# Kernel tuning notes

Hardware: AMD Instinct MI355X
Metric: run time of the kernel (lower is better)

The kernel has to match this reference:

```python
import jax, jax.numpy as jnp
import numpy as np

C = 128          # channels
L = 2            # num_layers
NA = 30000       # nodes of type 'a'
NB = 30000       # nodes of type 'b'
E = 150000       # edges per edge type
SEED_SIZE = 1024
EPS = 1e-5


def _ln(x, g, b):
    # LayerNorm over last dim (biased variance, eps=1e-5), matches nn.LayerNorm / PyG LayerNorm(mode='node')
    m = x.mean(-1, keepdims=True)
    v = ((x - m) ** 2).mean(-1, keepdims=True)
    return (x - m) * jax.lax.rsqrt(v + EPS) * g + b


def _seg_mean(msg, dst, n):
    # PyG aggr='mean': mean of incoming messages, 0 for isolated nodes
    s = jax.ops.segment_sum(msg, dst, num_segments=n)
    cnt = jax.ops.segment_sum(jnp.ones((dst.shape[0],), msg.dtype), dst, num_segments=n)
    return s / jnp.maximum(cnt, 1.0)[:, None]


def _prmp_conv(x_src, x_dst, edge, w1, b1, w2, b2, g, be, uw, ub):
    src, dst = edge[0], edge[1]
    xi = x_dst[dst]                                   # [E, C] dst feats per edge
    xj = x_src[src]                                   # [E, C] src feats per edge
    h = jax.nn.relu(jax.lax.stop_gradient(xi) @ w1 + b1)  # pred_mlp on detached x_i
    pred = h @ w2 + b2
    msg = _ln(xj - pred, g, be)                       # LayerNorm(residual) per edge
    agg = _seg_mean(msg, dst, x_dst.shape[0])         # mean aggregation to dst nodes
    return jax.nn.relu(jnp.concatenate([x_dst, agg], -1) @ uw + ub)  # update_mlp


def setup_inputs() -> dict:
    key = jax.random.key(0)
    ks = jax.random.split(key, 12)
    edge_ab = jnp.stack([jax.random.randint(ks[2], (E,), 0, NA, jnp.int32),
                         jax.random.randint(ks[3], (E,), 0, NB, jnp.int32)])
    edge_ba = jnp.stack([jax.random.randint(ks[4], (E,), 0, NB, jnp.int32),
                         jax.random.randint(ks[5], (E,), 0, NA, jnp.int32)])
    return {
        "x_a": jax.random.normal(ks[0], (NA, C), jnp.float32),
        "x_b": jax.random.normal(ks[1], (NB, C), jnp.float32),
        "edge_ab": edge_ab,
        "edge_ba": edge_ba,
        "pred_w1": jax.random.normal(ks[6], (L, 2, C, C), jnp.float32) * 0.05,
        "pred_b1": jnp.zeros((L, 2, C), jnp.float32),
        "pred_w2": jax.random.normal(ks[7], (L, 2, C, C), jnp.float32) * 0.05,
        "pred_b2": jnp.zeros((L, 2, C), jnp.float32),
        "msg_gamma": jnp.ones((L, 2, C), jnp.float32),
        "msg_beta": jnp.zeros((L, 2, C), jnp.float32),
        "upd_w": jax.random.normal(ks[8], (L, 2, 2 * C, C), jnp.float32) * 0.05,
        "upd_b": jnp.zeros((L, 2, C), jnp.float32),
        "node_gamma": jnp.ones((L, 2, C), jnp.float32),
        "node_beta": jnp.zeros((L, 2, C), jnp.float32),
        "head_w": jax.random.normal(ks[9], (C, 1), jnp.float32) * 0.05,
        "head_b": jnp.zeros((1,), jnp.float32),
        "seed_size": SEED_SIZE,
    }


def reference(x_a, x_b, edge_ab, edge_ba, pred_w1, pred_b1, pred_w2, pred_b2,
              msg_gamma, msg_beta, upd_w, upd_b, node_gamma, node_beta,
              head_w, head_b, seed_size):
    enc = lambda t: jnp.nan_to_num(t, nan=0.0, posinf=1.0, neginf=-1.0)
    x_a, x_b = enc(x_a), enc(x_b)
    for l in range(L):
        # edge type 0: a -> b ; edge type 1: b -> a (HeteroConv aggr='sum' is trivial: one conv per dst type)
        nb = _prmp_conv(x_a, x_b, edge_ab, pred_w1[l, 0], pred_b1[l, 0], pred_w2[l, 0], pred_b2[l, 0],
                        msg_gamma[l, 0], msg_beta[l, 0], upd_w[l, 0], upd_b[l, 0])
        na = _prmp_conv(x_b, x_a, edge_ba, pred_w1[l, 1], pred_b1[l, 1], pred_w2[l, 1], pred_b2[l, 1],
                        msg_gamma[l, 1], msg_beta[l, 1], upd_w[l, 1], upd_b[l, 1])
        na = jnp.nan_to_num(na, nan=0.0, posinf=10.0, neginf=-10.0)
        nb = jnp.nan_to_num(nb, nan=0.0, posinf=10.0, neginf=-10.0)
        x_a = jax.nn.relu(_ln(na, node_gamma[l, 0], node_beta[l, 0]))
        x_b = jax.nn.relu(_ln(nb, node_gamma[l, 1], node_beta[l, 1]))
    # head: single Linear(C -> 1) on the seed nodes of the entity table (type 'a')
    return x_a[:seed_size] @ head_w + head_b
```

## Files before the change

### kernel.cpp

```cpp
#include <hip/hip_runtime.h>

#define CC 128
#define ECAP 512

typedef __attribute__((ext_vector_type(8))) short bf16x8;
typedef __attribute__((ext_vector_type(4))) float f32x4;
#define MFMA16(a, b, c) __builtin_amdgcn_mfma_f32_16x16x32_bf16(a, b, c, 0, 0, 0)

__device__ __forceinline__ float enc_nan(float v) {
    if (v != v) return 0.f;
    if (v > 3.0e38f) return 1.f;
    if (v < -3.0e38f) return -1.f;
    return v;
}

__device__ __forceinline__ ushort f2bf(float x) {
    unsigned u = __builtin_bit_cast(unsigned, x);
    u += 0x7fff + ((u >> 16) & 1);
    return (ushort)(u >> 16);
}
__device__ __forceinline__ float bf2f(ushort h) {
    return __builtin_bit_cast(float, ((unsigned)h) << 16);
}

__device__ __forceinline__ int swz128(int row, int k) { return (row * 128 + k) ^ ((row & 7) << 3); }

__global__ __launch_bounds__(256)
void k_setup(const float* __restrict__ xa_in, ushort* __restrict__ xa,
             float2* __restrict__ stat_a, int NA,
             const float* __restrict__ xb_in, ushort* __restrict__ xb,
             float2* __restrict__ stat_b, int NB,
             const float* __restrict__ pw1, const float* __restrict__ pw2,
             const float* __restrict__ uw,
             ushort* __restrict__ w1t, ushort* __restrict__ w2t, ushort* __restrict__ uwt,
             const int* __restrict__ dst_b, int Eab, int* __restrict__ cnt_b,
             const int* __restrict__ dst_a, int Eba, int* __restrict__ cnt_a,
             int Ginit, int Gwcvt)
{
    const int b = blockIdx.x;
    const int tid = threadIdx.x;
    if (b < Ginit) {
        int row = b * 8 + (tid >> 5);
        int s = tid & 31;
        const float* xin; ushort* xo; float2* st;
        if (row < NA) { xin = xa_in; xo = xa; st = stat_a; }
        else {
            row -= NA;
            if (row >= NB) return;
            xin = xb_in; xo = xb; st = stat_b;
        }
        float4 v = *reinterpret_cast<const float4*>(xin + (size_t)row * CC + s * 4);
        ushort h0 = f2bf(enc_nan(v.x)), h1 = f2bf(enc_nan(v.y));
        ushort h2 = f2bf(enc_nan(v.z)), h3 = f2bf(enc_nan(v.w));
        *reinterpret_cast<ushort4*>(xo + (size_t)row * CC + s * 4) = make_ushort4(h0, h1, h2, h3);
        float r0 = bf2f(h0), r1 = bf2f(h1), r2 = bf2f(h2), r3 = bf2f(h3);
        float sm = (r0 + r1) + (r2 + r3);
        float sq = fmaf(r0, r0, fmaf(r1, r1, fmaf(r2, r2, r3 * r3)));
        #pragma unroll
        for (int m = 1; m < 32; m <<= 1) { sm += __shfl_xor(sm, m); sq += __shfl_xor(sq, m); }
        if (s == 0) st[row] = make_float2(sm, sq);
    } else if (b < Ginit + Gwcvt) {
        int i = (b - Ginit) * 256 + tid;
        int t = i >> 16;
        int r = i & 65535;
        if (r < 16384) {
            int k = r >> 7, c = r & 127;
            w1t[(size_t)t * 16384 + c * 128 + k] = f2bf(pw1[(size_t)t * 16384 + k * 128 + c]);
        } else if (r < 32768) {
            int rr = r - 16384;
            int k = rr >> 7, c = rr & 127;
            w2t[(size_t)t * 16384 + c * 128 + k] = f2bf(pw2[(size_t)t * 16384 + k * 128 + c]);
        } else {
            int rr = r - 32768;
            int k = rr >> 7, c = rr & 127;
            uwt[(size_t)t * 32768 + c * 256 + k] = f2bf(uw[(size_t)t * 32768 + k * 128 + c]);
        }
    } else {
        int i = (b - Ginit - Gwcvt) * 256 + tid;
        if (i < Eab) atomicAdd(&cnt_b[dst_b[i]], 1);
        else if (i - Eab < Eba) atomicAdd(&cnt_a[dst_a[i - Eab]], 1);
    }
}

__global__ __launch_bounds__(256)
void k_scanA(const int* __restrict__ cnt0, int* __restrict__ rowp0, int* __restrict__ part0,
             int n0, int Gb0,
             const int* __restrict__ cnt1, int* __restrict__ rowp1, int* __restrict__ part1, int n1)
{
    const int b = blockIdx.x;
    const bool sel = b < Gb0;
    const int* cnt = sel ? cnt0 : cnt1;
    int* rowp      = sel ? rowp0 : rowp1;
    int* part      = sel ? part0 : part1;
    const int n    = sel ? n0 : n1;
    const int bb   = sel ? b : b - Gb0;

    __shared__ int wsum[4];
    const int tid = threadIdx.x, lane = tid & 63, wid = tid >> 6;
    const int i = bb * 256 + tid;
    int v = (i < n) ? cnt[i] : 0;
    int incl = v;
    #pragma unroll
    for (int d = 1; d < 64; d <<= 1) {
        int t = __shfl_up(incl, d);
        if (lane >= d) incl += t;
    }
    if (lane == 63) wsum[wid] = incl;
    __syncthreads();
    int base = 0;
    #pragma unroll
    for (int j = 0; j < 4; ++j) if (j < wid) base += wsum[j];
    int excl = base + incl - v;
    if (i < n) rowp[i] = excl;
    if (tid == 255) part[bb] = excl + v;
}

__global__ __launch_bounds__(256)
void k_scanB(int* __restrict__ rowp0, const int* __restrict__ part0, int* __restrict__ off0,
             int n0, int Gb0,
             int* __restrict__ rowp1, const int* __restrict__ part1, int* __restrict__ off1, int n1)
{
    const int b = blockIdx.x;
    const bool sel = b < Gb0;
    int* rowp       = sel ? rowp0 : rowp1;
    const int* part = sel ? part0 : part1;
    int* off        = sel ? off0 : off1;
    const int n     = sel ? n0 : n1;
    const int bb    = sel ? b : b - Gb0;
    const int Gl    = sel ? Gb0 : (int)gridDim.x - Gb0;

    __shared__ int base_s;
    const int tid = threadIdx.x;
    if (tid < 64) {
        int s = 0;
        for (int j = tid; j < bb; j += 64) s += part[j];
        #pragma unroll
        for (int m = 1; m < 64; m <<= 1) s += __shfl_xor(s, m);
        if (tid == 0) base_s = s;
    }
    __syncthreads();
    const int base = base_s;
    const int i = bb * 256 + tid;
    if (i < n) {
        int r = rowp[i] + base;
        rowp[i] = r;
        off[i] = r;
    }
    if (bb == Gl - 1 && tid == 0) rowp[n] = base + part[bb];
}

__global__ __launch_bounds__(256)
void k_scatter_dual(const int* __restrict__ src_b, const int* __restrict__ dst_b, int Eab,
                    int* __restrict__ off_b, int* __restrict__ srcs_ab,
                    const int* __restrict__ src_a, const int* __restrict__ dst_a, int Eba,
                    int* __restrict__ off_a, int* __restrict__ srcs_ba)
{
    int i = blockIdx.x * 256 + threadIdx.x;
    if (i < Eab) {
        int p = atomicAdd(&off_b[dst_b[i]], 1);
        srcs_ab[p] = src_b[i];
    } else if (i - Eab < Eba) {
        int j = i - Eab;
        int p = atomicAdd(&off_a[dst_a[j]], 1);
        srcs_ba[p] = src_a[j];
    }
}

__device__ __forceinline__ void layer_body(
    char* smem,
    const ushort* __restrict__ xdst, const ushort* __restrict__ xsrc,
    const float2* __restrict__ stat_src,
    const int* __restrict__ rowp, const int* __restrict__ srcs,
    const ushort* __restrict__ w1t, const float* __restrict__ b1,
    const ushort* __restrict__ w2t, const float* __restrict__ b2,
    const float* __restrict__ mg, const float* __restrict__ mbt,
    const ushort* __restrict__ uwt, const float* __restrict__ ub,
    const float* __restrict__ ng, const float* __restrict__ nb,
    ushort* __restrict__ xout, float2* __restrict__ statOut, int N, int blk,
    const float* __restrict__ hw, const float* __restrict__ hb,
    float* __restrict__ hout, int headS)
{
    ushort* As = (ushort*)smem;
    ushort* Hs = (ushort*)(smem + 8192);
    ushort* P  = (ushort*)(smem + 16384);
    float (*os)[CC + 4] = (float(*)[CC + 4])(smem + 8192);
    int* sL   = (int*)(smem + 25088);
    int* shrp = (int*)(smem + 25088 + ECAP * 4);

    const int tid = threadIdx.x;
    const int base = blk * 32;
    const int w = tid >> 6, l = tid & 63;
    const int lr = l & 15, lg = l >> 4;

    if (tid < 33) {
        int nn = base + tid;
        shrp[tid] = rowp[nn < N ? nn : N];
    }
    {
        int row = tid >> 4, k0 = (tid & 15) << 3;
        int node = base + row;
        bf16x8 v0 = {};
        if (node < N)
            v0 = *reinterpret_cast<const bf16x8*>(xdst + (size_t)node * CC + k0);
        *reinterpret_cast<bf16x8*>(&As[swz128(row, k0)]) = v0;
    }
    const int jb0 = rowp[base];
    {
        int top = base + 32; if (top > N) top = N;
        const int je0 = rowp[top];
        int ec = je0 - jb0; if (ec > ECAP) ec = ECAP;
        if (tid < ec) sL[tid] = srcs[jb0 + tid];
    }
    __syncthreads();

    {
        f32x4 acc[2] = {};
        for (int kb = 0; kb < 4; ++kb) {
            int k = kb * 32 + lg * 8;
            bf16x8 a0 = *reinterpret_cast<const bf16x8*>(&As[swz128(lr, k)]);
            bf16x8 a1 = *reinterpret_cast<const bf16x8*>(&As[swz128(lr + 16, k)]);
            bf16x8 b0 = *reinterpret_cast<const bf16x8*>(&w1t[(size_t)(w * 16 + lr) * 128 + k]);
            acc[0] = MFMA16(a0, b0, acc[0]);
            acc[1] = MFMA16(a1, b0, acc[1]);
        }
        float bc = b1[w * 16 + lr];
        int col = w * 16 + lr;
        #pragma unroll
        for (int mi = 0; mi < 2; ++mi)
            #pragma unroll
            for (int j = 0; j < 4; ++j) {
                int row = mi * 16 + lg * 4 + j;
                Hs[swz128(row, col)] = f2bf(fmaxf(acc[mi][j] + bc, 0.f));
            }
    }
    __syncthreads();

    {
        f32x4 acc[2] = {};
        for (int kb = 0; kb < 4; ++kb) {
            int k = kb * 32 + lg * 8;
            bf16x8 a0 = *reinterpret_cast<const bf16x8*>(&Hs[swz128(lr, k)]);
            bf16x8 a1 = *reinterpret_cast<const bf16x8*>(&Hs[swz128(lr + 16, k)]);
            bf16x8 b0 = *reinterpret_cast<const bf16x8*>(&w2t[(size_t)(w * 16 + lr) * 128 + k]);
            acc[0] = MFMA16(a0, b0, acc[0]);
            acc[1] = MFMA16(a1, b0, acc[1]);
        }
        float bc = b2[w * 16 + lr];
        int col = w * 16 + lr;
        #pragma unroll
        for (int mi = 0; mi < 2; ++mi)
            #pragma unroll
            for (int j = 0; j < 4; ++j) {
                int row = mi * 16 + lg * 4 + j;
                P[row * CC + col] = f2bf(acc[mi][j] + bc);
            }
    }
    __syncthreads();

    {
        const int quarter = l >> 4;
        const int c = (l & 15) * 8;
        const float4 g0 = *reinterpret_cast<const float4*>(mg + c);
        const float4 g1 = *reinterpret_cast<const float4*>(mg + c + 4);
        const float4 e0 = *reinterpret_cast<const float4*>(mbt + c);
        const float4 e1 = *reinterpret_cast<const float4*>(mbt + c + 4);
        const float gv[8] = { g0.x, g0.y, g0.z, g0.w, g1.x, g1.y, g1.z, g1.w };
        const float bv[8] = { e0.x, e0.y, e0.z, e0.w, e1.x, e1.y, e1.z, e1.w };
        for (int i = 0; i < 4; ++i) {
            const int nl_ = w * 4 + i;
            const int d = base + nl_;
            if (d >= N) break;
            bf16x8 prb = *reinterpret_cast<const bf16x8*>(&P[nl_ * CC + c]);
            float pr[8];
            #pragma unroll
            for (int q = 0; q < 8; ++q) pr[q] = bf2f((ushort)prb[q]);
            float sp = 0.f, qp = 0.f;
            #pragma unroll
            for (int q = 0; q < 8; ++q) { sp += pr[q]; qp = fmaf(pr[q], pr[q], qp); }
            #pragma unroll
            for (int m = 1; m < 16; m <<= 1) { sp += __shfl_xor(sp, m); qp += __shfl_xor(qp, m); }
            const int jb = shrp[nl_], je = shrp[nl_ + 1];
            const int deg = je - jb;
            float a[8] = {};
            float rsum = 0.f, cmsum = 0.f;
            for (int j = jb + quarter; j < je; j += 4) {
                const int le = j - jb0;
                const int sidx = (le < ECAP) ? sL[le] : srcs[j];
                bf16x8 xb_ = *reinterpret_cast<const bf16x8*>(xsrc + (size_t)sidx * CC + c);
                const float2 st = stat_src[sidx];
                float xj[8];
                #pragma unroll
                for (int q = 0; q < 8; ++q) xj[q] = bf2f((ushort)xb_[q]);
                float dA = 0.f, dB = 0.f;
                #pragma unroll
                for (int q = 0; q < 4; ++q) dA = fmaf(xj[q], pr[q], dA);
                #pragma unroll
                for (int q = 4; q < 8; ++q) dB = fmaf(xj[q], pr[q], dB);
                float dot = dA + dB;
                #pragma unroll
                for (int m = 1; m < 16; m <<= 1) dot += __shfl_xor(dot, m);
                const float mean = (st.x - sp) * (1.f / 128.f);
                const float var = fmaf(-2.f, dot, st.y + qp) * (1.f / 128.f) - mean * mean;
                const float r = rsqrtf(var + 1e-5f);
                rsum += r;
                cmsum = fmaf(mean, r, cmsum);
                #pragma unroll
                for (int q = 0; q < 8; ++q) a[q] = fmaf(xj[q], r, a[q]);
            }
            #pragma unroll
            for (int q = 0; q < 8; ++q) { a[q] += __shfl_xor(a[q], 16); a[q] += __shfl_xor(a[q], 32); }
            rsum += __shfl_xor(rsum, 16);  rsum += __shfl_xor(rsum, 32);
            cmsum += __shfl_xor(cmsum, 16); cmsum += __shfl_xor(cmsum, 32);
            if (quarter == 0) {
                ushort o8[8];
                if (deg > 0) {
                    const float inv = 1.f / (float)deg;
                    #pragma unroll
                    for (int q = 0; q < 8; ++q)
                        o8[q] = f2bf(fmaf((a[q] - pr[q] * rsum - cmsum) * inv, gv[q], bv[q]));
                } else {
                    #pragma unroll
                    for (int q = 0; q < 8; ++q) o8[q] = 0;
                }
                *reinterpret_cast<bf16x8*>(&Hs[swz128(nl_, c)]) = *reinterpret_cast<bf16x8*>(&o8[0]);
            }
        }
    }
    __syncthreads();

    f32x4 acc[2] = {};
    for (int kb = 0; kb < 8; ++kb) {
        int k = kb * 32 + lg * 8;
        const ushort* Ab = (k < 128) ? As : Hs;
        int kl = k & 127;
        bf16x8 a0 = *reinterpret_cast<const bf16x8*>(&Ab[swz128(lr, kl)]);
        bf16x8 a1 = *reinterpret_cast<const bf16x8*>(&Ab[swz128(lr + 16, kl)]);
        bf16x8 b0 = *reinterpret_cast<const bf16x8*>(&uwt[(size_t)(w * 16 + lr) * 256 + k]);
        acc[0] = MFMA16(a0, b0, acc[0]);
        acc[1] = MFMA16(a1, b0, acc[1]);
    }
    __syncthreads();

    {
        float bc = ub[w * 16 + lr];
        int col = w * 16 + lr;
        #pragma unroll
        for (int mi = 0; mi < 2; ++mi)
            #pragma unroll
            for (int j = 0; j < 4; ++j) {
                int row = mi * 16 + lg * 4 + j;
                os[row][col] = fmaxf(acc[mi][j] + bc, 0.f);
            }
    }
    __syncthreads();

    const int nl = tid >> 4;
    const int cl = tid & 15;
    float vals[8];
    float sm = 0.f, sq = 0.f;
    #pragma unroll
    for (int t = 0; t < 8; ++t) {
        float u = os[nl][cl + 16 * t];
        vals[t] = u; sm += u; sq = fmaf(u, u, sq);
    }
    #pragma unroll
    for (int m = 1; m < 16; m <<= 1) { sm += __shfl_xor(sm, m); sq += __shfl_xor(sq, m); }
    float mean = sm * (1.f / 128.f);
    float var = sq * (1.f / 128.f) - mean * mean;
    float r = rsqrtf(var + 1e-5f);
    int node = base + nl;
    if (node < N) {
        float so = 0.f, sqo = 0.f, hsum = 0.f;
        bool doHead = (node < headS);
        #pragma unroll
        for (int t = 0; t < 8; ++t) {
            int cch = cl + 16 * t;
            float o = fmaxf(fmaf((vals[t] - mean) * r, ng[cch], nb[cch]), 0.f);
            ushort ob = f2bf(o);
            xout[(size_t)node * CC + cch] = ob;
            float orr = bf2f(ob);
            so += orr; sqo = fmaf(orr, orr, sqo);
            if (doHead) hsum = fmaf(o, hw[cch], hsum);
        }
        #pragma unroll
        for (int m = 1; m < 16; m <<= 1) { so += __shfl_xor(so, m); sqo += __shfl_xor(sqo, m); }
        if (doHead) {
            #pragma unroll
            for (int m = 1; m < 16; m <<= 1) hsum += __shfl_xor(hsum, m);
            if (cl == 0) hout[node] = hsum + hb[0];
        }
        if (cl == 0) statOut[node] = make_float2(so, sqo);
    }
}

__global__ __launch_bounds__(512)
void k_layer_dual(
    const ushort* __restrict__ xb_c, const ushort* __restrict__ xa_c,
    const float2* __restrict__ stat_a_c, const float2* __restrict__ stat_b_c,
    const int* __restrict__ rowp_b, const int* __restrict__ srcs_ab,
    const int* __restrict__ rowp_a, const int* __restrict__ srcs_ba,
    ushort* __restrict__ xb_n, ushort* __restrict__ xa_n,
    float2* __restrict__ stat_b_n, float2* __restrict__ stat_a_n,
    int NB, int NA, int GB,
    const ushort* __restrict__ w1t0, const float* __restrict__ b10,
    const ushort* __restrict__ w2t0, const float* __restrict__ b20,
    const float* __restrict__ mg0, const float* __restrict__ mb0,
    const ushort* __restrict__ uwt0, const float* __restrict__ ub0,
    const float* __restrict__ ng0, const float* __restrict__ nb0,
    const ushort* __restrict__ w1t1, const float* __restrict__ b11,
    const ushort* __restrict__ w2t1, const float* __restrict__ b21,
    const float* __restrict__ mg1, const float* __restrict__ mb1,
    const ushort* __restrict__ uwt1, const float* __restrict__ ub1,
    const float* __restrict__ ng1, const float* __restrict__ nb1,
    const float* __restrict__ hw, const float* __restrict__ hb,
    float* __restrict__ hout, int headS)
{
    __shared__ __align__(16) char smem[25088 + ECAP * 4 + 144];
    if ((int)blockIdx.x < GB)
        layer_body(smem, xb_c, xa_c, stat_a_c, rowp_b, srcs_ab,
                   w1t0, b10, w2t0, b20, mg0, mb0, uwt0, ub0, ng0, nb0,
                   xb_n, stat_b_n, NB, blockIdx.x, hw, hb, hout, 0);
    else
        layer_body(smem, xa_c, xb_c, stat_b_c, rowp_a, srcs_ba,
                   w1t1, b11, w2t1, b21, mg1, mb1, uwt1, ub1, ng1, nb1,
                   xa_n, stat_a_n, NA, blockIdx.x - GB, hw, hb, hout, headS);
}

extern "C" void kernel_launch(void* const* d_in, const int* in_sizes, int n_in,
                              void* d_out, int out_size, void* d_ws, size_t ws_size,
                              hipStream_t stream)
{
    const float* x_a_in = (const float*)d_in[0];
    const float* x_b_in = (const float*)d_in[1];
    const int*   e_ab   = (const int*)d_in[2];
    const int*   e_ba   = (const int*)d_in[3];
    const float* pw1    = (const float*)d_in[4];
    const float* pb1    = (const float*)d_in[5];
    const float* pw2    = (const float*)d_in[6];
    const float* pb2    = (const float*)d_in[7];
    const float* mgam   = (const float*)d_in[8];
    const float* mbet   = (const float*)d_in[9];
    const float* uw     = (const float*)d_in[10];
    const float* ubias  = (const float*)d_in[11];
    const float* ngam   = (const float*)d_in[12];
    const float* nbet   = (const float*)d_in[13];
    const float* hw     = (const float*)d_in[14];
    const float* hb     = (const float*)d_in[15];

    const int NA  = in_sizes[0] / CC;
    const int NB  = in_sizes[1] / CC;
    const int Eab = in_sizes[2] / 2;
    const int Eba = in_sizes[3] / 2;

    float* ws = (float*)d_ws;
    size_t off = 0;
    ushort* xa0 = (ushort*)(ws + off); off += (size_t)NA * CC / 2;
    ushort* xa1 = (ushort*)(ws + off); off += (size_t)NA * CC / 2;
    ushort* xb0 = (ushort*)(ws + off); off += (size_t)NB * CC / 2;
    ushort* xb1 = (ushort*)(ws + off); off += (size_t)NB * CC / 2;
    float2* sa0 = (float2*)(ws + off); off += (size_t)NA * 2;
    float2* sa1 = (float2*)(ws + off); off += (size_t)NA * 2;
    float2* sb0 = (float2*)(ws + off); off += (size_t)NB * 2;
    float2* sb1 = (float2*)(ws + off); off += (size_t)NB * 2;
    ushort* w1t = (ushort*)(ws + off); off += 4 * 16384 / 2;
    ushort* w2t = (ushort*)(ws + off); off += 4 * 16384 / 2;
    ushort* uwt = (ushort*)(ws + off); off += 4 * 32768 / 2;
    int* iw = (int*)(ws + off);
    size_t ioff = 0;
    int* cnt_b   = iw + ioff; ioff += NB;
    int* cnt_a   = iw + ioff; ioff += NA;
    int* rowp_b  = iw + ioff; ioff += NB + 1;
    int* rowp_a  = iw + ioff; ioff += NA + 1;
    int* off_b   = iw + ioff; ioff += NB;
    int* off_a   = iw + ioff; ioff += NA;
    int* srcs_ab = iw + ioff; ioff += Eab;
    int* srcs_ba = iw + ioff; ioff += Eba;
    const int GbS = (NB + 255) / 256, GaS = (NA + 255) / 256;
    int* part_b  = iw + ioff; ioff += GbS;
    int* part_a  = iw + ioff; ioff += GaS;

    const int GB = (NB + 31) / 32, GA = (NA + 31) / 32;
    const int Ginit = (NA + NB + 7) / 8;
    const int Gwcvt = 1024;
    const int Ghist = (Eab + Eba + 255) / 256;

    hipMemsetAsync(cnt_b, 0, (size_t)(NB + NA) * sizeof(int), stream);
    k_setup<<<dim3(Ginit + Gwcvt + Ghist), dim3(256), 0, stream>>>(
        x_a_in, xa0, sa0, NA, x_b_in, xb0, sb0, NB,
        pw1, pw2, uw, w1t, w2t, uwt,
        e_ab + Eab, Eab, cnt_b, e_ba + Eba, Eba, cnt_a,
        Ginit, Gwcvt);
    k_scanA<<<dim3(GbS + GaS), dim3(256), 0, stream>>>(
        cnt_b, rowp_b, part_b, NB, GbS, cnt_a, rowp_a, part_a, NA);
    k_scanB<<<dim3(GbS + GaS), dim3(256), 0, stream>>>(
        rowp_b, part_b, off_b, NB, GbS, rowp_a, part_a, off_a, NA);
    k_scatter_dual<<<dim3((Eab + Eba + 255) / 256), dim3(256), 0, stream>>>(
        e_ab, e_ab + Eab, Eab, off_b, srcs_ab,
        e_ba, e_ba + Eba, Eba, off_a, srcs_ba);

    ushort* xac = xa0; ushort* xan = xa1;
    ushort* xbc = xb0; ushort* xbn = xb1;
    float2* sac = sa0; float2* san = sa1;
    float2* sbc = sb0; float2* sbn = sb1;

    for (int lyr = 0; lyr < 2; ++lyr) {
        int t0 = lyr * 2 + 0;
        int t1 = lyr * 2 + 1;
        int headS = (lyr == 1) ? out_size : 0;

        k_layer_dual<<<dim3(GB + GA), dim3(512), 0, stream>>>(
            xbc, xac, sac, sbc,
            rowp_b, srcs_ab, rowp_a, srcs_ba,
            xbn, xan, sbn, san,
            NB, NA, GB,
            w1t + (size_t)t0 * 16384, pb1 + t0 * CC, w2t + (size_t)t0 * 16384, pb2 + t0 * CC,
            mgam + t0 * CC, mbet + t0 * CC,
            uwt + (size_t)t0 * 32768, ubias + t0 * CC, ngam + t0 * CC, nbet + t0 * CC,
            w1t + (size_t)t1 * 16384, pb1 + t1 * CC, w2t + (size_t)t1 * 16384, pb2 + t1 * CC,
            mgam + t1 * CC, mbet + t1 * CC,
            uwt + (size_t)t1 * 32768, ubias + t1 * CC, ngam + t1 * CC, nbet + t1 * CC,
            hw, hb, (float*)d_out, headS);

        ushort* t;
        t = xac; xac = xan; xan = t;
        t = xbc; xbc = xbn; xbn = t;
        float2* s;
        s = sac; sac = san; san = s;
        s = sbc; sbc = sbn; sbn = s;
    }
}
```

Before: 207.9 us.

## Sort destination nodes by in-degree to balance per-block edge work

Adds a degree histogram, a scan and a permutation pass that reorder destination nodes by in-degree. The CSR is built in that sorted order and each layer block processes 32 nodes of similar degree, reading and writing node rows through the permutation. The aim is to cut load imbalance and ECAP overflow variance within blocks. In exchange it adds three small kernels and indirect, scattered row loads and stores in the layer kernel.

```diff
diff --git a/kernel.cpp b/kernel.cpp
--- a/kernel.cpp
+++ b/kernel.cpp
@@ -83,6 +83,55 @@
 }
 
 __global__ __launch_bounds__(256)
+void k_dhist(const int* __restrict__ cnt_b, int NB, const int* __restrict__ cnt_a, int NA,
+             int* __restrict__ dh)
+{
+    int i = blockIdx.x * 256 + threadIdx.x;
+    if (i < NB) {
+        int d = cnt_b[i]; if (d > 63) d = 63;
+        atomicAdd(&dh[d], 1);
+    } else if (i - NB < NA) {
+        int d = cnt_a[i - NB]; if (d > 63) d = 63;
+        atomicAdd(&dh[64 + d], 1);
+    }
+}
+
+__global__ __launch_bounds__(128)
+void k_dscan(const int* __restrict__ dh, int* __restrict__ dbase)
+{
+    const int tid = threadIdx.x, lane = tid & 63;
+    int v = dh[tid];
+    int incl = v;
+    #pragma unroll
+    for (int d = 1; d < 64; d <<= 1) {
+        int t = __shfl_up(incl, d);
+        if (lane >= d) incl += t;
+    }
+    dbase[tid] = incl - v;
+}
+
+__global__ __launch_bounds__(256)
+void k_dperm(const int* __restrict__ cnt_b, int NB, int* __restrict__ dbase,
+             int* __restrict__ perm_b, int* __restrict__ rank_b, int* __restrict__ cnt_sb,
+             const int* __restrict__ cnt_a, int NA,
+             int* __restrict__ perm_a, int* __restrict__ rank_a, int* __restrict__ cnt_sa)
+{
+    int i = blockIdx.x * 256 + threadIdx.x;
+    if (i < NB) {
+        int deg = cnt_b[i];
+        int d = deg > 63 ? 63 : deg;
+        int r = atomicAdd(&dbase[d], 1);
+        perm_b[r] = i; rank_b[i] = r; cnt_sb[r] = deg;
+    } else if (i - NB < NA) {
+        int j = i - NB;
+        int deg = cnt_a[j];
+        int d = deg > 63 ? 63 : deg;
+        int r = atomicAdd(&dbase[64 + d], 1);
+        perm_a[r] = j; rank_a[j] = r; cnt_sa[r] = deg;
+    }
+}
+
+__global__ __launch_bounds__(256)
 void k_scanA(const int* __restrict__ cnt0, int* __restrict__ rowp0, int* __restrict__ part0,
              int n0, int Gb0,
              const int* __restrict__ cnt1, int* __restrict__ rowp1, int* __restrict__ part1, int n1)
@@ -151,17 +200,17 @@
 
 __global__ __launch_bounds__(256)
 void k_scatter_dual(const int* __restrict__ src_b, const int* __restrict__ dst_b, int Eab,
-                    int* __restrict__ off_b, int* __restrict__ srcs_ab,
+                    const int* __restrict__ rank_b, int* __restrict__ off_b, int* __restrict__ srcs_ab,
                     const int* __restrict__ src_a, const int* __restrict__ dst_a, int Eba,
-                    int* __restrict__ off_a, int* __restrict__ srcs_ba)
+                    const int* __restrict__ rank_a, int* __restrict__ off_a, int* __restrict__ srcs_ba)
 {
     int i = blockIdx.x * 256 + threadIdx.x;
     if (i < Eab) {
-        int p = atomicAdd(&off_b[dst_b[i]], 1);
+        int p = atomicAdd(&off_b[rank_b[dst_b[i]]], 1);
         srcs_ab[p] = src_b[i];
     } else if (i - Eab < Eba) {
         int j = i - Eab;
-        int p = atomicAdd(&off_a[dst_a[j]], 1);
+        int p = atomicAdd(&off_a[rank_a[dst_a[j]]], 1);
         srcs_ba[p] = src_a[j];
     }
 }
@@ -169,7 +218,7 @@
 __device__ __forceinline__ void layer_body(
     char* smem,
     const ushort* __restrict__ xdst, const ushort* __restrict__ xsrc,
-    const float2* __restrict__ stat_src,
+    const float2* __restrict__ stat_src, const int* __restrict__ perm,
     const int* __restrict__ rowp, const int* __restrict__ srcs,
     const ushort* __restrict__ w1t, const float* __restrict__ b1,
     const ushort* __restrict__ w2t, const float* __restrict__ b2,
@@ -198,10 +247,12 @@
     }
     {
         int row = tid >> 4, k0 = (tid & 15) << 3;
-        int node = base + row;
+        int pnode = base + row;
         bf16x8 v0 = {};
-        if (node < N)
-            v0 = *reinterpret_cast<const bf16x8*>(xdst + (size_t)node * CC + k0);
+        if (pnode < N) {
+            int anode = perm[pnode];
+            v0 = *reinterpret_cast<const bf16x8*>(xdst + (size_t)anode * CC + k0);
+        }
         *reinterpret_cast<bf16x8*>(&As[swz128(row, k0)]) = v0;
     }
     const int jb0 = rowp[base];
@@ -368,16 +419,17 @@
     float mean = sm * (1.f / 128.f);
     float var = sq * (1.f / 128.f) - mean * mean;
     float r = rsqrtf(var + 1e-5f);
-    int node = base + nl;
-    if (node < N) {
+    int pnode = base + nl;
+    if (pnode < N) {
+        const int anode = perm[pnode];
         float so = 0.f, sqo = 0.f, hsum = 0.f;
-        bool doHead = (node < headS);
+        bool doHead = (anode < headS);
         #pragma unroll
         for (int t = 0; t < 8; ++t) {
             int cch = cl + 16 * t;
             float o = fmaxf(fmaf((vals[t] - mean) * r, ng[cch], nb[cch]), 0.f);
             ushort ob = f2bf(o);
-            xout[(size_t)node * CC + cch] = ob;
+            xout[(size_t)anode * CC + cch] = ob;
             float orr = bf2f(ob);
             so += orr; sqo = fmaf(orr, orr, sqo);
             if (doHead) hsum = fmaf(o, hw[cch], hsum);
@@ -387,9 +439,9 @@
         if (doHead) {
             #pragma unroll
             for (int m = 1; m < 16; m <<= 1) hsum += __shfl_xor(hsum, m);
-            if (cl == 0) hout[node] = hsum + hb[0];
-        }
-        if (cl == 0) statOut[node] = make_float2(so, sqo);
+            if (cl == 0) hout[anode] = hsum + hb[0];
+        }
+        if (cl == 0) statOut[anode] = make_float2(so, sqo);
     }
 }
 
@@ -397,6 +449,7 @@
 void k_layer_dual(
     const ushort* __restrict__ xb_c, const ushort* __restrict__ xa_c,
     const float2* __restrict__ stat_a_c, const float2* __restrict__ stat_b_c,
+    const int* __restrict__ perm_b, const int* __restrict__ perm_a,
     const int* __restrict__ rowp_b, const int* __restrict__ srcs_ab,
     const int* __restrict__ rowp_a, const int* __restrict__ srcs_ba,
     ushort* __restrict__ xb_n, ushort* __restrict__ xa_n,
@@ -417,11 +470,11 @@
 {
     __shared__ __align__(16) char smem[25088 + ECAP * 4 + 144];
     if ((int)blockIdx.x < GB)
-        layer_body(smem, xb_c, xa_c, stat_a_c, rowp_b, srcs_ab,
+        layer_body(smem, xb_c, xa_c, stat_a_c, perm_b, rowp_b, srcs_ab,
                    w1t0, b10, w2t0, b20, mg0, mb0, uwt0, ub0, ng0, nb0,
                    xb_n, stat_b_n, NB, blockIdx.x, hw, hb, hout, 0);
     else
-        layer_body(smem, xa_c, xb_c, stat_b_c, rowp_a, srcs_ba,
+        layer_body(smem, xa_c, xb_c, stat_b_c, perm_a, rowp_a, srcs_ba,
                    w1t1, b11, w2t1, b21, mg1, mb1, uwt1, ub1, ng1, nb1,
                    xa_n, stat_a_n, NA, blockIdx.x - GB, hw, hb, hout, headS);
 }
@@ -469,6 +522,7 @@
     size_t ioff = 0;
     int* cnt_b   = iw + ioff; ioff += NB;
     int* cnt_a   = iw + ioff; ioff += NA;
+    int* dh      = iw + ioff; ioff += 128;
     int* rowp_b  = iw + ioff; ioff += NB + 1;
     int* rowp_a  = iw + ioff; ioff += NA + 1;
     int* off_b   = iw + ioff; ioff += NB;
@@ -478,25 +532,38 @@
     const int GbS = (NB + 255) / 256, GaS = (NA + 255) / 256;
     int* part_b  = iw + ioff; ioff += GbS;
     int* part_a  = iw + ioff; ioff += GaS;
+    int* dbase   = iw + ioff; ioff += 128;
+    int* perm_b  = iw + ioff; ioff += NB;
+    int* rank_b  = iw + ioff; ioff += NB;
+    int* perm_a  = iw + ioff; ioff += NA;
+    int* rank_a  = iw + ioff; ioff += NA;
+    int* cnt_sb  = iw + ioff; ioff += NB;
+    int* cnt_sa  = iw + ioff; ioff += NA;
 
     const int GB = (NB + 31) / 32, GA = (NA + 31) / 32;
     const int Ginit = (NA + NB + 7) / 8;
     const int Gwcvt = 1024;
     const int Ghist = (Eab + Eba + 255) / 256;
-
-    hipMemsetAsync(cnt_b, 0, (size_t)(NB + NA) * sizeof(int), stream);
+    const int Gn    = (NA + NB + 255) / 256;
+
+    hipMemsetAsync(cnt_b, 0, (size_t)(NB + NA + 128) * sizeof(int), stream);
     k_setup<<<dim3(Ginit + Gwcvt + Ghist), dim3(256), 0, stream>>>(
         x_a_in, xa0, sa0, NA, x_b_in, xb0, sb0, NB,
         pw1, pw2, uw, w1t, w2t, uwt,
         e_ab + Eab, Eab, cnt_b, e_ba + Eba, Eba, cnt_a,
         Ginit, Gwcvt);
+    k_dhist<<<dim3(Gn), dim3(256), 0, stream>>>(cnt_b, NB, cnt_a, NA, dh);
+    k_dscan<<<dim3(1), dim3(128), 0, stream>>>(dh, dbase);
+    k_dperm<<<dim3(Gn), dim3(256), 0, stream>>>(
+        cnt_b, NB, dbase, perm_b, rank_b, cnt_sb,
+        cnt_a, NA, perm_a, rank_a, cnt_sa);
     k_scanA<<<dim3(GbS + GaS), dim3(256), 0, stream>>>(
-        cnt_b, rowp_b, part_b, NB, GbS, cnt_a, rowp_a, part_a, NA);
+        cnt_sb, rowp_b, part_b, NB, GbS, cnt_sa, rowp_a, part_a, NA);
     k_scanB<<<dim3(GbS + GaS), dim3(256), 0, stream>>>(
         rowp_b, part_b, off_b, NB, GbS, rowp_a, part_a, off_a, NA);
     k_scatter_dual<<<dim3((Eab + Eba + 255) / 256), dim3(256), 0, stream>>>(
-        e_ab, e_ab + Eab, Eab, off_b, srcs_ab,
-        e_ba, e_ba + Eba, Eba, off_a, srcs_ba);
+        e_ab, e_ab + Eab, Eab, rank_b, off_b, srcs_ab,
+        e_ba, e_ba + Eba, Eba, rank_a, off_a, srcs_ba);
 
     ushort* xac = xa0; ushort* xan = xa1;
     ushort* xbc = xb0; ushort* xbn = xb1;
@@ -510,6 +577,7 @@
 
         k_layer_dual<<<dim3(GB + GA), dim3(512), 0, stream>>>(
             xbc, xac, sac, sbc,
+            perm_b, perm_a,
             rowp_b, srcs_ab, rowp_a, srcs_ba,
             xbn, xan, sbn, san,
             NB, NA, GB,
```

Result: slower. 455.1 us (+118.9%).
